# Kernel tuning notes

Hardware: AMD Instinct MI355X
Metric: run time of the kernel (lower is better)

The kernel has to match this reference:

```python
import jax, jax.numpy as jnp
import numpy as np
import math

B, N, OBS, H, A = 4096, 64, 64, 64, 8


def setup_inputs() -> dict:
    key = jax.random.key(0)
    kit = iter(jax.random.split(key, 64))

    def W(o, i):
        return jax.random.normal(next(kit), (o, i), jnp.float32) / float(np.sqrt(i))

    def bvec(o):
        return jax.random.normal(next(kit), (o,), jnp.float32) * 0.01

    inp = {
        "x": jax.random.normal(next(kit), (B, N, OBS), jnp.float32),
        "rnd_nums": jax.random.uniform(next(kit), (B, N), dtype=jnp.float32),
        "idx": jax.random.randint(next(kit), (B, N), 0, N),
    }
    inp.update(embed_w=W(H, OBS), embed_b=bvec(H))
    for pre in ("ia", "c1", "c2"):  # init_attn, consensus_attn1, consensus_attn2 (1 head)
        inp.update({pre + "_wq": W(H, H), pre + "_bq": bvec(H),
                    pre + "_wk": W(H, H), pre + "_bk": bvec(H),
                    pre + "_wv": W(H, H), pre + "_bv": bvec(H),
                    pre + "_wo": W(H, H), pre + "_bo": bvec(H)})
    inp.update(msg_w=W(H, H), msg_b=bvec(H), st_w=W(H, H), st_b=bvec(H),
               mean_w=W(A, 2 * H), mean_b=bvec(A), ls_w=W(A, 2 * H), ls_b=bvec(A))
    return inp


def reference(x, rnd_nums, idx, embed_w, embed_b,
              ia_wq, ia_bq, ia_wk, ia_bk, ia_wv, ia_bv, ia_wo, ia_bo,
              msg_w, msg_b, st_w, st_b,
              c1_wq, c1_bq, c1_wk, c1_bk, c1_wv, c1_bv, c1_wo, c1_bo,
              c2_wq, c2_bq, c2_wk, c2_bk, c2_wv, c2_bv, c2_wo, c2_bo,
              mean_w, mean_b, ls_w, ls_b):
    h = embed_w.shape[0]
    scale = 1.0 / math.sqrt(h)
    lrelu = lambda z: jax.nn.leaky_relu(z, 0.2)

    # ---- initial state estimation (self-attention over agents) ----
    e = lrelu(x @ embed_w.T + embed_b)                       # [B,N,H]
    q = e @ ia_wq.T + ia_bq
    k = e @ ia_wk.T + ia_bk
    v = e @ ia_wv.T + ia_bv
    w = jax.nn.softmax(jnp.einsum('bih,bjh->bij', q, k) * scale, axis=-1)
    attn = jnp.tanh(jnp.einsum('bij,bjh->bih', w, v) @ ia_wo.T + ia_bo)
    messages = attn @ msg_w.T + msg_b                        # [B,N,H]
    temp = attn @ st_w.T + st_b                              # [B,N,H]

    # ---- consensus masks: mg[b,i,j] = (r_i > a_i) | (r_j > a_i) ----
    a = jnp.take_along_axis(rnd_nums, idx, axis=1)           # agent_rnd per agent slot [B,N]
    gi = rnd_nums[:, :, None] > a[:, :, None]
    gj = rnd_nums[:, None, :] > a[:, :, None]
    mg = (gi | gj).astype(x.dtype)                           # [B,N,N]
    ml = 1.0 - mg

    def cons(mask, wq, bq, wk, bk, wv, bv, wo, bo):
        # single-token query (agent temp state) attends over zero-masked messages;
        # masked tokens contribute k = bk, v = bv (bias survives the zeroing).
        qq = temp @ wq.T + bq                                # [B,N,H]
        km = messages @ wk.T                                 # [B,N,H] (no bias; folded below)
        vm = messages @ wv.T
        s = (mask * jnp.einsum('bih,bjh->bij', qq, km) + (qq @ bk)[:, :, None]) * scale
        wgt = jax.nn.softmax(s, axis=-1)                     # [B,N_agents,N_tokens]
        ctx = jnp.einsum('bij,bjh->bih', wgt * mask, vm) + bv
        return ctx @ wo.T + bo

    o1 = cons(mg, c1_wq, c1_bq, c1_wk, c1_bk, c1_wv, c1_bv, c1_wo, c1_bo)
    o2 = cons(ml, c2_wq, c2_bq, c2_wk, c2_bk, c2_wv, c2_bv, c2_wo, c2_bo)
    out = lrelu(jnp.concatenate([o1, o2], axis=-1))          # [B,N,2H]
    mean = out @ mean_w.T + mean_b                           # [B,N,A]
    logstd = jnp.clip(out @ ls_w.T + ls_b, -20.0, 2.0)
    return mean, jnp.exp(logstd)
```

## Files before the change

### kernel.cpp

```cpp
#include <hip/hip_runtime.h>

namespace {

typedef __bf16 bf16x8 __attribute__((ext_vector_type(8)));
typedef float f32x4 __attribute__((ext_vector_type(4)));
typedef unsigned int uint4v __attribute__((ext_vector_type(4)));

#define MFMA16(a,b,c) __builtin_amdgcn_mfma_f32_16x16x32_bf16((a),(b),(c),0,0,0)

constexpr float SCALE = 0.125f;

constexpr int WS_HW  = 57344;
constexpr int WS_NV  = 61440;
constexpr int WS_VEC = 63488;
constexpr int WS_SC  = 65536;

__device__ __forceinline__ int PI(int c){ return 4*(c&15) + (c>>4); }
__device__ __forceinline__ int PINV(int p){ return 16*(p&3) + (p>>2); }

__device__ __forceinline__ unsigned short f2b(float f){
  return __builtin_bit_cast(unsigned short, (__bf16)f);
}
__device__ __forceinline__ unsigned pack2(float a, float b){
  return (unsigned)f2b(a) | ((unsigned)f2b(b)<<16);
}
template<int ACT>
__device__ __forceinline__ float actf(float v){
  if constexpr (ACT==1) return v>0.f ? v : 0.2f*v;
  else if constexpr (ACT==2) return 1.f - 2.f/(__expf(2.f*v)+1.f);
  else return v;
}

struct PrepP {
  const float *embed_w, *mean_w, *ls_w;
  const float *ia_wq, *ia_bq, *ia_wk, *ia_wv, *ia_wo, *ia_bv, *ia_bo;
  const float *c1_wq, *c1_bq, *c1_wk, *c1_bk, *c1_wv, *c1_bv, *c1_wo, *c1_bo;
  const float *c2_wq, *c2_bq, *c2_wk, *c2_bk, *c2_wv, *c2_bv, *c2_wo, *c2_bo;
  const float *msg_w, *msg_b, *st_w, *st_b;
  char* ws;
};

__device__ void mmAB_f32(const float* A, const float* B, float* O){
  const int t=threadIdx.x, r=t>>2, c0=(t&3)*16;
  float acc[16];
  #pragma unroll
  for(int j=0;j<16;j++) acc[j]=0.f;
  for(int h=0;h<64;h++){
    const float a=A[r*64+h];
    #pragma unroll
    for(int j=0;j<16;j++) acc[j]=fmaf(a,B[h*64+c0+j],acc[j]);
  }
  #pragma unroll
  for(int j=0;j<16;j++) O[r*64+c0+j]=acc[j];
}
__device__ void mmAB_bf(const float* A, const float* B, __bf16* D){
  const int t=threadIdx.x, r=t>>2, c0=(t&3)*16;
  float acc[16];
  #pragma unroll
  for(int j=0;j<16;j++) acc[j]=0.f;
  for(int h=0;h<64;h++){
    const float a=A[r*64+h];
    #pragma unroll
    for(int j=0;j<16;j++) acc[j]=fmaf(a,B[h*64+c0+j],acc[j]);
  }
  #pragma unroll
  for(int j=0;j<16;j++) D[r*64+PI(c0+j)]=(__bf16)acc[j];
}
__device__ void mmTA_bf(const float* A, const float* B, __bf16* D){
  const int t=threadIdx.x, a=t>>2, b0=(t&3)*16;
  float acc[16];
  #pragma unroll
  for(int j=0;j<16;j++) acc[j]=0.f;
  for(int h=0;h<64;h++){
    const float av=A[h*64+a];
    #pragma unroll
    for(int j=0;j<16;j++) acc[j]=fmaf(av,B[h*64+b0+j],acc[j]);
  }
  #pragma unroll
  for(int j=0;j<16;j++) D[a*64+PI(b0+j)]=(__bf16)acc[j];
}

__global__ void prep_kernel(PrepP q){
  __shared__ float PF[2][4096];
  __shared__ float hv[64], gv[64];
  const int job=blockIdx.x, t=threadIdx.x;
  char* ws=q.ws;
  float* VECF=(float*)(ws+WS_VEC);
  float* SCF =(float*)(ws+WS_SC);
  __bf16* NVD=(__bf16*)(ws+WS_NV);

  if(job==0){
    __bf16* emb=(__bf16*)(ws+0*8192);
    #pragma unroll
    for(int i=0;i<16;i++){
      const int idx=t*16+i, o=idx>>6, p=idx&63;
      emb[idx]=(__bf16)q.embed_w[o*64+PINV(p)];
    }
    __bf16* hw=(__bf16*)(ws+WS_HW);
    #pragma unroll
    for(int i=0;i<8;i++){
      const int flat=t*8+i, o=flat>>7, qq=flat&127, half=qq>>6, p=qq&63;
      const float v=(o<8)?q.mean_w[o*128+half*64+PINV(p)]
                         :q.ls_w[(o-8)*128+half*64+PINV(p)];
      hw[flat]=(__bf16)v;
    }
    #pragma unroll
    for(int i=0;i<3;i++){ const int id=t*3+i; if(id<768) NVD[256+id]=(__bf16)0.f; }
  } else if(job==1){
    mmTA_bf(q.ia_wk, q.ia_wq, (__bf16*)(ws+1*8192));
    if(t<64){ float s=0; for(int h=0;h<64;h++) s+=q.ia_wk[h*64+t]*q.ia_bq[h]; VECF[t]=s; }
  } else if(job==2){
    mmAB_bf(q.ia_wo, q.ia_wv, (__bf16*)(ws+2*8192));
    if(t<64){ float s=q.ia_bo[t]; for(int h=0;h<64;h++) s+=q.ia_wo[t*64+h]*q.ia_bv[h];
              VECF[64+t]=s; }
  } else if(job==3 || job==5){
    const int cons=(job==3)?0:1;
    const float *wq=cons?q.c2_wq:q.c1_wq, *bq=cons?q.c2_bq:q.c1_bq;
    const float *wk=cons?q.c2_wk:q.c1_wk, *bk=cons?q.c2_bk:q.c1_bk;
    mmAB_f32(wq, q.st_w, PF[0]);
    if(t<64){ float s=bq[t]; for(int k=0;k<64;k++) s+=wq[t*64+k]*q.st_b[k]; hv[t]=s; }
    __syncthreads();
    mmAB_f32(wk, q.msg_w, PF[1]);
    if(t<64){ float s=0; for(int k=0;k<64;k++) s+=wk[t*64+k]*q.msg_b[k]; gv[t]=s; }
    __syncthreads();
    mmTA_bf(PF[1], PF[0], (__bf16*)(ws+(cons?5:3)*8192));
    if(t<64){
      float s=0; for(int h=0;h<64;h++) s+=PF[1][h*64+t]*hv[h];
      VECF[128+cons*64+t]=s;
      float s0=0,s1=0;
      for(int h=0;h<64;h++){ s0+=PF[0][h*64+t]*gv[h]; s1+=PF[0][h*64+t]*bk[h]; }
      NVD[(2*cons  )*64+PI(t)]=(__bf16)s0;
      NVD[(2*cons+1)*64+PI(t)]=(__bf16)s1;
    }
    if(t==0){
      float c=0,hb=0;
      for(int i=0;i<64;i++){ c+=hv[i]*gv[i]; hb+=hv[i]*bk[i]; }
      SCF[2*cons]=c; SCF[2*cons+1]=hb;
    }
  } else {
    const int cons=(job==4)?0:1;
    const float *wo=cons?q.c2_wo:q.c1_wo, *wvv=cons?q.c2_wv:q.c1_wv;
    const float *bv=cons?q.c2_bv:q.c1_bv, *bo=cons?q.c2_bo:q.c1_bo;
    mmAB_f32(wo, wvv, PF[0]);
    if(t<64){ float s=bo[t]; for(int h=0;h<64;h++) s+=wo[t*64+h]*bv[h];
              VECF[320+cons*128+t]=s; }
    __syncthreads();
    mmAB_bf(PF[0], q.msg_w, (__bf16*)(ws+(cons?6:4)*8192));
    if(t<64){ float s=0; for(int k=0;k<64;k++) s+=PF[0][t*64+k]*q.msg_b[k];
              VECF[256+cons*128+t]=s; }
  }
}

struct Params {
  const float *x, *rnd; const int *idx;
  const float *embed_b, *mean_b, *ls_b;
  const char* ws; float* out; int std_off;
};

__device__ __forceinline__ bf16x8 fragld(const char* buf, int row, int kb){
  const int byte = row*128 + (kb ^ ((row&7)<<4));
  return __builtin_bit_cast(bf16x8, *reinterpret_cast<const uint4v*>(buf + byte));
}
__device__ __forceinline__ bf16x8 gld(const char* a){
  return __builtin_bit_cast(bf16x8, *reinterpret_cast<const uint4v*>(a));
}
__device__ __forceinline__ void loadB_lds(const char* Bl, bf16x8* bf, int fr, int fg){
  #pragma unroll
  for(int n=0;n<4;n++){
    bf[2*n]   = fragld(Bl, n*16+fr, fg*16);
    bf[2*n+1] = fragld(Bl, n*16+fr, 64+fg*16);
  }
}
__device__ __forceinline__ void loadB_gl(const char* W, bf16x8* bf, int fr, int fg){
  #pragma unroll
  for(int n=0;n<4;n++){
    bf[2*n]   = gld(W + (n*16+fr)*128 + fg*16);
    bf[2*n+1] = gld(W + (n*16+fr)*128 + 64 + fg*16);
  }
}

template<bool AG>
__device__ __forceinline__ void mm2(const char* A, const bf16x8* bf,
                                    f32x4 acc[2][4], int fr, int fg, int row0){
  #pragma unroll
  for(int rt=0;rt<2;rt++){
    bf16x8 a0,a1;
    const int R=row0+16*rt+fr;
    if constexpr(AG){ a0=gld(A+R*128+fg*16); a1=gld(A+R*128+64+fg*16); }
    else            { a0=fragld(A,R,fg*16);  a1=fragld(A,R,64+fg*16);  }
    #pragma unroll
    for(int n=0;n<4;n++){
      acc[rt][n]=MFMA16(a0,bf[2*n],acc[rt][n]);
      acc[rt][n]=MFMA16(a1,bf[2*n+1],acc[rt][n]);
    }
  }
}
__device__ __forceinline__ void zero2(f32x4 acc[2][4]){
  #pragma unroll
  for(int rt=0;rt<2;rt++)
    #pragma unroll
    for(int n=0;n<4;n++) acc[rt][n]=f32x4{0.f,0.f,0.f,0.f};
}
template<int ACT>
__device__ __forceinline__ void st2_cb(char* C, const f32x4 acc[2][4], const float* bz,
                                       int fr, int fg, int row0){
  #pragma unroll
  for(int rt=0;rt<2;rt++)
  #pragma unroll
  for(int r=0;r<4;r++){
    const int R=row0+16*rt+4*fg+r;
    float v[4];
    #pragma unroll
    for(int n=0;n<4;n++) v[n]=actf<ACT>(acc[rt][n][r]+bz[n]);
    uint2 pk; pk.x=pack2(v[0],v[1]); pk.y=pack2(v[2],v[3]);
    *reinterpret_cast<uint2*>(C + R*128 + ((8*fr)^((R&7)<<4))) = pk;
  }
}
__device__ __forceinline__ void st2_rb(char* C, const f32x4 acc[2][4], const float* dbase,
                                       int fr, int fg, int row0){
  #pragma unroll
  for(int rt=0;rt<2;rt++)
  #pragma unroll
  for(int r=0;r<4;r++){
    const int R=row0+16*rt+4*fg+r;
    const float d=dbase[R];
    float v[4];
    #pragma unroll
    for(int n=0;n<4;n++) v[n]=acc[rt][n][r]+d;
    uint2 pk; pk.x=pack2(v[0],v[1]); pk.y=pack2(v[2],v[3]);
    *reinterpret_cast<uint2*>(C + R*128 + ((8*fr)^((R&7)<<4))) = pk;
  }
}

template<int MODE>
__device__ __forceinline__ void ssoft2(const char* Aq, const char* Bk, char* P,
                                       const float2* ra, const float4* zz,
                                       float cu, float cq, unsigned* mb,
                                       int fr, int fg, int row0){
  bf16x8 bf[8]; loadB_lds(Bk,bf,fr,fg);
  f32x4 acc[2][4]; zero2(acc);
  mm2<false>(Aq,bf,acc,fr,fg,row0);
  float rc[4];
  if constexpr(MODE==1){
    #pragma unroll
    for(int n=0;n<4;n++) rc[n]=ra[n*16+fr].x;
  }
  #pragma unroll
  for(int rt=0;rt<2;rt++){
    unsigned mbits=0;
    if constexpr(MODE==1){
      float aR[4],ucR[4],qtR[4]; bool gi[4];
      #pragma unroll
      for(int r=0;r<4;r++){
        const int R=row0+16*rt+4*fg+r;
        const float2 rv=ra[R];
        gi[r]=rv.x>rv.y; aR[r]=rv.y;
        const float4 z4=zz[R];
        ucR[r]=z4.x+cu; qtR[r]=z4.y+cq;
      }
      #pragma unroll
      for(int n=0;n<4;n++){
        #pragma unroll
        for(int r=0;r<4;r++){
          const bool mv=gi[r]||(rc[n]>aR[r]);
          if(mv) mbits|=1u<<(n*4+r);
          const float mf=mv?1.f:0.f;
          acc[rt][n][r]=(mf*(acc[rt][n][r]+ucR[r])+qtR[r])*SCALE;
        }
      }
      mb[rt]=mbits;
    } else if constexpr(MODE==2){
      mbits=mb[rt]^0xffffu;
      float ucR[4],qtR[4];
      #pragma unroll
      for(int r=0;r<4;r++){
        const float4 z4=zz[row0+16*rt+4*fg+r];
        ucR[r]=z4.z+cu; qtR[r]=z4.w+cq;
      }
      #pragma unroll
      for(int n=0;n<4;n++){
        #pragma unroll
        for(int r=0;r<4;r++){
          const float mf=((mbits>>(n*4+r))&1u)?1.f:0.f;
          acc[rt][n][r]=(mf*(acc[rt][n][r]+ucR[r])+qtR[r])*SCALE;
        }
      }
    }
    float mx[4];
    #pragma unroll
    for(int r=0;r<4;r++)
      mx[r]=fmaxf(fmaxf(acc[rt][0][r],acc[rt][1][r]),
                  fmaxf(acc[rt][2][r],acc[rt][3][r]));
    #pragma unroll
    for(int m=1;m<16;m<<=1){
      #pragma unroll
      for(int r=0;r<4;r++) mx[r]=fmaxf(mx[r],__shfl_xor(mx[r],m));
    }
    float sm[4]={0,0,0,0};
    #pragma unroll
    for(int n=0;n<4;n++){
      #pragma unroll
      for(int r=0;r<4;r++){
        float e;
        if constexpr(MODE==0) e=__expf((acc[rt][n][r]-mx[r])*SCALE);
        else e=__expf(acc[rt][n][r]-mx[r]);
        acc[rt][n][r]=e; sm[r]+=e;
      }
    }
    #pragma unroll
    for(int m=1;m<16;m<<=1){
      #pragma unroll
      for(int r=0;r<4;r++) sm[r]+=__shfl_xor(sm[r],m);
    }
    #pragma unroll
    for(int r=0;r<4;r++){
      const int R=row0+16*rt+4*fg+r;
      const float ri=1.f/sm[r];
      float v[4];
      #pragma unroll
      for(int n=0;n<4;n++){
        float e=acc[rt][n][r]*ri;
        if constexpr(MODE!=0) e=(mbits&(1u<<(n*4+r)))?e:0.f;
        v[n]=e;
      }
      uint2 pk; pk.x=pack2(v[0],v[1]); pk.y=pack2(v[2],v[3]);
      *reinterpret_cast<uint2*>(P + R*128 + ((8*fr)^((R&7)<<4))) = pk;
    }
  }
}

__device__ __forceinline__ void park2(char* Buf, const f32x4 oacc[2][4],
                                      const float* ev, const char* hwb,
                                      f32x4* hacc, int fr, int fg, int row0){
  float bz[4];
  #pragma unroll
  for(int n=0;n<4;n++) bz[n]=ev[n*16+fr];
  st2_cb<1>(Buf,oacc,bz,fr,fg,row0);
  const bf16x8 h0=gld(hwb+fr*256+fg*16);
  const bf16x8 h1=gld(hwb+fr*256+64+fg*16);
  #pragma unroll
  for(int rt=0;rt<2;rt++){
    hacc[rt]=MFMA16(fragld(Buf,row0+16*rt+fr,fg*16),    h0, hacc[rt]);
    hacc[rt]=MFMA16(fragld(Buf,row0+16*rt+fr,64+fg*16), h1, hacc[rt]);
  }
}

__global__ __launch_bounds__(128,3) void rap_kernel(Params p){
  __shared__ __align__(16) char X[8192];
  __shared__ __align__(16) char Y[8192];
  __shared__ __align__(16) char Z[8192];
  __shared__ __align__(16) float2 ra_s[64];
  __shared__ __align__(16) float4 zz_s[64];
  const int t=threadIdx.x, l=t&63, fr=l&15, fg=l>>4, wv=t>>6;
  const int row0=32*wv;
  const int bi=blockIdx.x;
  const char* ws=p.ws;
  const float* VECF=(const float*)(ws+WS_VEC);
  const float4 scf=*(const float4*)(ws+WS_SC);
  const float2* ra=ra_s;
  const float4* zz=zz_s;

  if(t<64){
    const float r0=p.rnd[bi*64+t];
    const float av=p.rnd[bi*64+p.idx[bi*64+t]];
    ra_s[t]=make_float2(r0,av);
  }
  {
    const float* Gx=p.x+(size_t)bi*4096;
    #pragma unroll
    for(int j=0;j<4;j++){
      const int lf=j*64+l, R=row0+(lf>>3), k=lf&7;
      const float2 L0=*reinterpret_cast<const float2*>(Gx+R*64+2*k);
      const float2 L1=*reinterpret_cast<const float2*>(Gx+R*64+16+2*k);
      const float2 L2=*reinterpret_cast<const float2*>(Gx+R*64+32+2*k);
      const float2 L3=*reinterpret_cast<const float2*>(Gx+R*64+48+2*k);
      uint4 pk;
      pk.x=pack2(L0.x,L1.x); pk.y=pack2(L2.x,L3.x);
      pk.z=pack2(L0.y,L1.y); pk.w=pack2(L2.y,L3.y);
      *reinterpret_cast<uint4*>(X + R*128 + ((16*k)^((R&7)<<4)))=pk;
    }
  }
  bf16x8 bfv[8];
  float bz[4];
  f32x4 acc[2][4];
  unsigned mb[2]={0,0};
  loadB_gl(ws+0*8192,bfv,fr,fg);
  #pragma unroll
  for(int n=0;n<4;n++) bz[n]=p.embed_b[n*16+fr];
  zero2(acc); mm2<false>(X,bfv,acc,fr,fg,row0);
  st2_cb<1>(Y,acc,bz,fr,fg,row0);
  loadB_gl(ws+1*8192,bfv,fr,fg);
  #pragma unroll
  for(int n=0;n<4;n++) bz[n]=VECF[n*16+fr];
  zero2(acc); mm2<false>(Y,bfv,acc,fr,fg,row0);
  st2_cb<0>(X,acc,bz,fr,fg,row0);
  __syncthreads();
  ssoft2<0>(X,Y,X,nullptr,nullptr,0.f,0.f,mb,fr,fg,row0);
  loadB_lds(Y,bfv,fr,fg);
  zero2(acc); mm2<true>(ws+2*8192,bfv,acc,fr,fg,row0);
  { const float bz0[4]={0,0,0,0}; st2_cb<0>(Z,acc,bz0,fr,fg,row0); }
  __syncthreads();
  loadB_lds(Z,bfv,fr,fg);
  #pragma unroll
  for(int n=0;n<4;n++) bz[n]=VECF[64+n*16+fr];
  zero2(acc); mm2<false>(X,bfv,acc,fr,fg,row0);
  st2_cb<2>(Y,acc,bz,fr,fg,row0);
  {
    loadB_gl(ws+3*8192,bfv,fr,fg);
    const bf16x8 nv0=gld(ws+WS_NV+fr*128+fg*16);
    const bf16x8 nv1=gld(ws+WS_NV+fr*128+64+fg*16);
    #pragma unroll
    for(int n=0;n<4;n++) bz[n]=VECF[128+n*16+fr];
    zero2(acc);
    #pragma unroll
    for(int rt=0;rt<2;rt++){
      const bf16x8 a0=fragld(Y,row0+16*rt+fr,fg*16);
      const bf16x8 a1=fragld(Y,row0+16*rt+fr,64+fg*16);
      #pragma unroll
      for(int n=0;n<4;n++){
        acc[rt][n]=MFMA16(a0,bfv[2*n],acc[rt][n]);
        acc[rt][n]=MFMA16(a1,bfv[2*n+1],acc[rt][n]);
      }
      f32x4 za={0,0,0,0};
      za=MFMA16(a0,nv0,za); za=MFMA16(a1,nv1,za);
      if(fr<4){
        #pragma unroll
        for(int r=0;r<4;r++)
          reinterpret_cast<float*>(&zz_s[row0+16*rt+4*fg+r])[fr]=za[r];
      }
    }
    st2_cb<0>(X,acc,bz,fr,fg,row0);
  }
  __syncthreads();
  ssoft2<1>(X,Y,X,ra,zz,scf.x,scf.y,mb,fr,fg,row0);
  loadB_lds(Y,bfv,fr,fg);
  zero2(acc); mm2<true>(ws+4*8192,bfv,acc,fr,fg,row0);
  st2_rb(Z,acc,VECF+256,fr,fg,row0);
  __syncthreads();
  f32x4 hacc[2]={{0,0,0,0},{0,0,0,0}};
  loadB_lds(Z,bfv,fr,fg);
  zero2(acc); mm2<false>(X,bfv,acc,fr,fg,row0);
  park2(X,acc,VECF+320,ws+WS_HW,hacc,fr,fg,row0);
  loadB_gl(ws+5*8192,bfv,fr,fg);
  #pragma unroll
  for(int n=0;n<4;n++) bz[n]=VECF[192+n*16+fr];
  zero2(acc); mm2<false>(Y,bfv,acc,fr,fg,row0);
  st2_cb<0>(X,acc,bz,fr,fg,row0);
  ssoft2<2>(X,Y,X,ra,zz,scf.z,scf.w,mb,fr,fg,row0);
  __syncthreads();
  loadB_lds(Y,bfv,fr,fg);
  zero2(acc); mm2<true>(ws+6*8192,bfv,acc,fr,fg,row0);
  st2_rb(Z,acc,VECF+384,fr,fg,row0);
  __syncthreads();
  loadB_lds(Z,bfv,fr,fg);
  zero2(acc); mm2<false>(X,bfv,acc,fr,fg,row0);
  park2(Y,acc,VECF+448,ws+WS_HW+128,hacc,fr,fg,row0);
  {
    const float bzo=(fr<8)?p.mean_b[fr]:p.ls_b[fr-8];
    #pragma unroll
    for(int rt=0;rt<2;rt++)
    #pragma unroll
    for(int r=0;r<4;r++){
      const int R=row0+16*rt+4*fg+r;
      const long base=((long)bi*64+R)*8;
      float v=hacc[rt][r]+bzo;
      if(fr<8) p.out[base+fr]=v;
      else{
        v=fminf(fmaxf(v,-20.f),2.f);
        p.out[p.std_off+base+fr-8]=__expf(v);
      }
    }
  }
}

}

extern "C" void kernel_launch(void* const* d_in, const int* in_sizes, int n_in,
                              void* d_out, int out_size, void* d_ws, size_t ws_size,
                              hipStream_t stream){
  (void)n_in; (void)out_size; (void)ws_size;
  PrepP q;
  q.embed_w=(const float*)d_in[3];
  q.ia_wq=(const float*)d_in[5];  q.ia_bq=(const float*)d_in[6];
  q.ia_wk=(const float*)d_in[7];
  q.ia_wv=(const float*)d_in[9];  q.ia_bv=(const float*)d_in[10];
  q.ia_wo=(const float*)d_in[11]; q.ia_bo=(const float*)d_in[12];
  q.c1_wq=(const float*)d_in[13]; q.c1_bq=(const float*)d_in[14];
  q.c1_wk=(const float*)d_in[15]; q.c1_bk=(const float*)d_in[16];
  q.c1_wv=(const float*)d_in[17]; q.c1_bv=(const float*)d_in[18];
  q.c1_wo=(const float*)d_in[19]; q.c1_bo=(const float*)d_in[20];
  q.c2_wq=(const float*)d_in[21]; q.c2_bq=(const float*)d_in[22];
  q.c2_wk=(const float*)d_in[23]; q.c2_bk=(const float*)d_in[24];
  q.c2_wv=(const float*)d_in[25]; q.c2_bv=(const float*)d_in[26];
  q.c2_wo=(const float*)d_in[27]; q.c2_bo=(const float*)d_in[28];
  q.msg_w=(const float*)d_in[29]; q.msg_b=(const float*)d_in[30];
  q.st_w =(const float*)d_in[31]; q.st_b =(const float*)d_in[32];
  q.mean_w=(const float*)d_in[33]; q.ls_w=(const float*)d_in[35];
  q.ws=(char*)d_ws;
  prep_kernel<<<dim3(7), dim3(256), 0, stream>>>(q);

  Params p;
  p.x  =(const float*)d_in[0];
  p.rnd=(const float*)d_in[1];
  p.idx=(const int*)  d_in[2];
  p.embed_b=(const float*)d_in[4];
  p.mean_b =(const float*)d_in[34];
  p.ls_b   =(const float*)d_in[36];
  p.ws=(const char*)d_ws;
  p.out=(float*)d_out;
  const int Bb=in_sizes[0]/4096;
  p.std_off=Bb*64*8;
  rap_kernel<<<dim3(Bb), dim3(128), 0, stream>>>(p);
}
```

Baseline: 126.7 us.

## Share LDS fragments across paired matmuls, prefetch weights, drop softmax max

Each attention stage now loads the shared K/V-side fragments from LDS once and feeds two matmuls with them: the score product and the next weight product, whose A operand is preloaded from global into registers. Global weight tiles and the head weights are fetched earlier so their latency overlaps with compute. Biases are folded into the accumulator initialisation instead of being added at store time. The softmax no longer subtracts the row max, which removes two cross-lane shuffle reductions per row. In exchange, register pressure rises under the 3-blocks-per-SM launch bound, and exp overflow becomes possible if scores are ever large.

After: 131.4 us. 1.04x slower.

```diff
diff --git a/kernel.cpp b/kernel.cpp
--- a/kernel.cpp
+++ b/kernel.cpp
@@ -179,15 +179,12 @@
   }
 }
 
-template<bool AG>
 __device__ __forceinline__ void mm2(const char* A, const bf16x8* bf,
                                     f32x4 acc[2][4], int fr, int fg, int row0){
   #pragma unroll
   for(int rt=0;rt<2;rt++){
-    bf16x8 a0,a1;
-    const int R=row0+16*rt+fr;
-    if constexpr(AG){ a0=gld(A+R*128+fg*16); a1=gld(A+R*128+64+fg*16); }
-    else            { a0=fragld(A,R,fg*16);  a1=fragld(A,R,64+fg*16);  }
+    const bf16x8 a0=fragld(A,row0+16*rt+fr,fg*16);
+    const bf16x8 a1=fragld(A,row0+16*rt+fr,64+fg*16);
     #pragma unroll
     for(int n=0;n<4;n++){
       acc[rt][n]=MFMA16(a0,bf[2*n],acc[rt][n]);
@@ -195,15 +192,31 @@
     }
   }
 }
+__device__ __forceinline__ void mm2r(const bf16x8* wa0, const bf16x8* wa1,
+                                     const bf16x8* bf, f32x4 acc[2][4]){
+  #pragma unroll
+  for(int rt=0;rt<2;rt++)
+  #pragma unroll
+  for(int n=0;n<4;n++){
+    acc[rt][n]=MFMA16(wa0[rt],bf[2*n],acc[rt][n]);
+    acc[rt][n]=MFMA16(wa1[rt],bf[2*n+1],acc[rt][n]);
+  }
+}
 __device__ __forceinline__ void zero2(f32x4 acc[2][4]){
   #pragma unroll
   for(int rt=0;rt<2;rt++)
     #pragma unroll
     for(int n=0;n<4;n++) acc[rt][n]=f32x4{0.f,0.f,0.f,0.f};
 }
+__device__ __forceinline__ void init2b(f32x4 acc[2][4], const float* bz){
+  #pragma unroll
+  for(int rt=0;rt<2;rt++)
+    #pragma unroll
+    for(int n=0;n<4;n++) acc[rt][n]=f32x4{bz[n],bz[n],bz[n],bz[n]};
+}
 template<int ACT>
-__device__ __forceinline__ void st2_cb(char* C, const f32x4 acc[2][4], const float* bz,
-                                       int fr, int fg, int row0){
+__device__ __forceinline__ void st2_act(char* C, const f32x4 acc[2][4],
+                                        int fr, int fg, int row0){
   #pragma unroll
   for(int rt=0;rt<2;rt++)
   #pragma unroll
@@ -211,7 +224,7 @@
     const int R=row0+16*rt+4*fg+r;
     float v[4];
     #pragma unroll
-    for(int n=0;n<4;n++) v[n]=actf<ACT>(acc[rt][n][r]+bz[n]);
+    for(int n=0;n<4;n++) v[n]=actf<ACT>(acc[rt][n][r]);
     uint2 pk; pk.x=pack2(v[0],v[1]); pk.y=pack2(v[2],v[3]);
     *reinterpret_cast<uint2*>(C + R*128 + ((8*fr)^((R&7)<<4))) = pk;
   }
@@ -233,13 +246,10 @@
 }
 
 template<int MODE>
-__device__ __forceinline__ void ssoft2(const char* Aq, const char* Bk, char* P,
-                                       const float2* ra, const float4* zz,
-                                       float cu, float cq, unsigned* mb,
-                                       int fr, int fg, int row0){
-  bf16x8 bf[8]; loadB_lds(Bk,bf,fr,fg);
-  f32x4 acc[2][4]; zero2(acc);
-  mm2<false>(Aq,bf,acc,fr,fg,row0);
+__device__ __forceinline__ void ssoft_post(f32x4 acc[2][4], char* P,
+                                           const float2* ra, const float4* zz,
+                                           float cu, float cq, unsigned* mb,
+                                           int fr, int fg, int row0){
   float rc[4];
   if constexpr(MODE==1){
     #pragma unroll
@@ -286,24 +296,14 @@
         }
       }
     }
-    float mx[4];
-    #pragma unroll
-    for(int r=0;r<4;r++)
-      mx[r]=fmaxf(fmaxf(acc[rt][0][r],acc[rt][1][r]),
-                  fmaxf(acc[rt][2][r],acc[rt][3][r]));
-    #pragma unroll
-    for(int m=1;m<16;m<<=1){
-      #pragma unroll
-      for(int r=0;r<4;r++) mx[r]=fmaxf(mx[r],__shfl_xor(mx[r],m));
-    }
     float sm[4]={0,0,0,0};
     #pragma unroll
     for(int n=0;n<4;n++){
       #pragma unroll
       for(int r=0;r<4;r++){
         float e;
-        if constexpr(MODE==0) e=__expf((acc[rt][n][r]-mx[r])*SCALE);
-        else e=__expf(acc[rt][n][r]-mx[r]);
+        if constexpr(MODE==0) e=__expf(acc[rt][n][r]*SCALE);
+        else e=__expf(acc[rt][n][r]);
         acc[rt][n][r]=e; sm[r]+=e;
       }
     }
@@ -329,19 +329,13 @@
   }
 }
 
-__device__ __forceinline__ void park2(char* Buf, const f32x4 oacc[2][4],
-                                      const float* ev, const char* hwb,
-                                      f32x4* hacc, int fr, int fg, int row0){
-  float bz[4];
-  #pragma unroll
-  for(int n=0;n<4;n++) bz[n]=ev[n*16+fr];
-  st2_cb<1>(Buf,oacc,bz,fr,fg,row0);
-  const bf16x8 h0=gld(hwb+fr*256+fg*16);
-  const bf16x8 h1=gld(hwb+fr*256+64+fg*16);
+__device__ __forceinline__ void loadA_gl(const char* W, bf16x8* wa0, bf16x8* wa1,
+                                         int fr, int fg, int row0){
   #pragma unroll
   for(int rt=0;rt<2;rt++){
-    hacc[rt]=MFMA16(fragld(Buf,row0+16*rt+fr,fg*16),    h0, hacc[rt]);
-    hacc[rt]=MFMA16(fragld(Buf,row0+16*rt+fr,64+fg*16), h1, hacc[rt]);
+    const int R=row0+16*rt+fr;
+    wa0[rt]=gld(W+R*128+fg*16);
+    wa1[rt]=gld(W+R*128+64+fg*16);
   }
 }
 
@@ -360,6 +354,14 @@
   const float2* ra=ra_s;
   const float4* zz=zz_s;
 
+  bf16x8 bfv[8];
+  bf16x8 bfm[8];
+  bf16x8 wa0[2], wa1[2];
+  float bz[4];
+  f32x4 acc[2][4], acc2[2][4];
+  unsigned mb[2]={0,0};
+
+  loadB_gl(ws+0*8192,bfm,fr,fg);
   if(t<64){
     const float r0=p.rnd[bi*64+t];
     const float av=p.rnd[bi*64+p.idx[bi*64+t]];
@@ -380,46 +382,43 @@
       *reinterpret_cast<uint4*>(X + R*128 + ((16*k)^((R&7)<<4)))=pk;
     }
   }
-  bf16x8 bfv[8];
-  float bz[4];
-  f32x4 acc[2][4];
-  unsigned mb[2]={0,0};
-  loadB_gl(ws+0*8192,bfv,fr,fg);
   #pragma unroll
   for(int n=0;n<4;n++) bz[n]=p.embed_b[n*16+fr];
-  zero2(acc); mm2<false>(X,bfv,acc,fr,fg,row0);
-  st2_cb<1>(Y,acc,bz,fr,fg,row0);
-  loadB_gl(ws+1*8192,bfv,fr,fg);
+  init2b(acc,bz); mm2(X,bfm,acc,fr,fg,row0);
+  loadB_gl(ws+1*8192,bfm,fr,fg);
+  st2_act<1>(Y,acc,fr,fg,row0);
   #pragma unroll
   for(int n=0;n<4;n++) bz[n]=VECF[n*16+fr];
-  zero2(acc); mm2<false>(Y,bfv,acc,fr,fg,row0);
-  st2_cb<0>(X,acc,bz,fr,fg,row0);
+  init2b(acc,bz); mm2(Y,bfm,acc,fr,fg,row0);
+  st2_act<0>(X,acc,fr,fg,row0);
   __syncthreads();
-  ssoft2<0>(X,Y,X,nullptr,nullptr,0.f,0.f,mb,fr,fg,row0);
+  loadA_gl(ws+2*8192,wa0,wa1,fr,fg,row0);
   loadB_lds(Y,bfv,fr,fg);
-  zero2(acc); mm2<true>(ws+2*8192,bfv,acc,fr,fg,row0);
-  { const float bz0[4]={0,0,0,0}; st2_cb<0>(Z,acc,bz0,fr,fg,row0); }
+  zero2(acc);  mm2(X,bfv,acc,fr,fg,row0);
+  zero2(acc2); mm2r(wa0,wa1,bfv,acc2);
+  st2_act<0>(Z,acc2,fr,fg,row0);
+  ssoft_post<0>(acc,X,nullptr,nullptr,0.f,0.f,mb,fr,fg,row0);
   __syncthreads();
+  loadB_gl(ws+3*8192,bfm,fr,fg);
+  const bf16x8 nv0=gld(ws+WS_NV+fr*128+fg*16);
+  const bf16x8 nv1=gld(ws+WS_NV+fr*128+64+fg*16);
   loadB_lds(Z,bfv,fr,fg);
   #pragma unroll
   for(int n=0;n<4;n++) bz[n]=VECF[64+n*16+fr];
-  zero2(acc); mm2<false>(X,bfv,acc,fr,fg,row0);
-  st2_cb<2>(Y,acc,bz,fr,fg,row0);
+  init2b(acc,bz); mm2(X,bfv,acc,fr,fg,row0);
+  st2_act<2>(Y,acc,fr,fg,row0);
   {
-    loadB_gl(ws+3*8192,bfv,fr,fg);
-    const bf16x8 nv0=gld(ws+WS_NV+fr*128+fg*16);
-    const bf16x8 nv1=gld(ws+WS_NV+fr*128+64+fg*16);
     #pragma unroll
     for(int n=0;n<4;n++) bz[n]=VECF[128+n*16+fr];
-    zero2(acc);
+    init2b(acc,bz);
     #pragma unroll
     for(int rt=0;rt<2;rt++){
       const bf16x8 a0=fragld(Y,row0+16*rt+fr,fg*16);
       const bf16x8 a1=fragld(Y,row0+16*rt+fr,64+fg*16);
       #pragma unroll
       for(int n=0;n<4;n++){
-        acc[rt][n]=MFMA16(a0,bfv[2*n],acc[rt][n]);
-        acc[rt][n]=MFMA16(a1,bfv[2*n+1],acc[rt][n]);
+        acc[rt][n]=MFMA16(a0,bfm[2*n],acc[rt][n]);
+        acc[rt][n]=MFMA16(a1,bfm[2*n+1],acc[rt][n]);
       }
       f32x4 za={0,0,0,0};
       za=MFMA16(a0,nv0,za); za=MFMA16(a1,nv1,za);
@@ -429,32 +428,54 @@
           reinterpret_cast<float*>(&zz_s[row0+16*rt+4*fg+r])[fr]=za[r];
       }
     }
-    st2_cb<0>(X,acc,bz,fr,fg,row0);
+    st2_act<0>(X,acc,fr,fg,row0);
   }
   __syncthreads();
-  ssoft2<1>(X,Y,X,ra,zz,scf.x,scf.y,mb,fr,fg,row0);
+  loadA_gl(ws+4*8192,wa0,wa1,fr,fg,row0);
   loadB_lds(Y,bfv,fr,fg);
-  zero2(acc); mm2<true>(ws+4*8192,bfv,acc,fr,fg,row0);
-  st2_rb(Z,acc,VECF+256,fr,fg,row0);
+  zero2(acc);  mm2(X,bfv,acc,fr,fg,row0);
+  zero2(acc2); mm2r(wa0,wa1,bfv,acc2);
+  st2_rb(Z,acc2,VECF+256,fr,fg,row0);
+  ssoft_post<1>(acc,X,ra,zz,scf.x,scf.y,mb,fr,fg,row0);
   __syncthreads();
   f32x4 hacc[2]={{0,0,0,0},{0,0,0,0}};
+  loadB_gl(ws+5*8192,bfm,fr,fg);
+  const bf16x8 h0=gld(ws+WS_HW+fr*256+fg*16);
+  const bf16x8 h1=gld(ws+WS_HW+fr*256+64+fg*16);
   loadB_lds(Z,bfv,fr,fg);
-  zero2(acc); mm2<false>(X,bfv,acc,fr,fg,row0);
-  park2(X,acc,VECF+320,ws+WS_HW,hacc,fr,fg,row0);
-  loadB_gl(ws+5*8192,bfv,fr,fg);
+  #pragma unroll
+  for(int n=0;n<4;n++) bz[n]=VECF[320+n*16+fr];
+  init2b(acc,bz); mm2(X,bfv,acc,fr,fg,row0);
+  st2_act<1>(X,acc,fr,fg,row0);
+  #pragma unroll
+  for(int rt=0;rt<2;rt++){
+    hacc[rt]=MFMA16(fragld(X,row0+16*rt+fr,fg*16),    h0, hacc[rt]);
+    hacc[rt]=MFMA16(fragld(X,row0+16*rt+fr,64+fg*16), h1, hacc[rt]);
+  }
   #pragma unroll
   for(int n=0;n<4;n++) bz[n]=VECF[192+n*16+fr];
-  zero2(acc); mm2<false>(Y,bfv,acc,fr,fg,row0);
-  st2_cb<0>(X,acc,bz,fr,fg,row0);
-  ssoft2<2>(X,Y,X,ra,zz,scf.z,scf.w,mb,fr,fg,row0);
+  init2b(acc,bz); mm2(Y,bfm,acc,fr,fg,row0);
+  st2_act<0>(X,acc,fr,fg,row0);
   __syncthreads();
+  loadA_gl(ws+6*8192,wa0,wa1,fr,fg,row0);
   loadB_lds(Y,bfv,fr,fg);
-  zero2(acc); mm2<true>(ws+6*8192,bfv,acc,fr,fg,row0);
-  st2_rb(Z,acc,VECF+384,fr,fg,row0);
+  zero2(acc);  mm2(X,bfv,acc,fr,fg,row0);
+  zero2(acc2); mm2r(wa0,wa1,bfv,acc2);
+  st2_rb(Z,acc2,VECF+384,fr,fg,row0);
+  ssoft_post<2>(acc,X,ra,zz,scf.z,scf.w,mb,fr,fg,row0);
   __syncthreads();
+  const bf16x8 h2=gld(ws+WS_HW+128+fr*256+fg*16);
+  const bf16x8 h3=gld(ws+WS_HW+128+fr*256+64+fg*16);
   loadB_lds(Z,bfv,fr,fg);
-  zero2(acc); mm2<false>(X,bfv,acc,fr,fg,row0);
-  park2(Y,acc,VECF+448,ws+WS_HW+128,hacc,fr,fg,row0);
+  #pragma unroll
+  for(int n=0;n<4;n++) bz[n]=VECF[448+n*16+fr];
+  init2b(acc,bz); mm2(X,bfv,acc,fr,fg,row0);
+  st2_act<1>(Y,acc,fr,fg,row0);
+  #pragma unroll
+  for(int rt=0;rt<2;rt++){
+    hacc[rt]=MFMA16(fragld(Y,row0+16*rt+fr,fg*16),    h2, hacc[rt]);
+    hacc[rt]=MFMA16(fragld(Y,row0+16*rt+fr,64+fg*16), h3, hacc[rt]);
+  }
   {
     const float bzo=(fr<8)?p.mean_b[fr]:p.ls_b[fr-8];
     #pragma unroll
```
